# Optimization experiments

Measured on AMD Instinct MI355X. Metric: run time of the kernel, lower is better.

## Reference

```python
import jax, jax.numpy as jnp
import numpy as np

K_DIM = 1024
HEADS = 16


def setup_inputs() -> dict:
    key = jax.random.key(0)
    kx, kw1, kb1, kw2, kb2 = jax.random.split(key, 5)
    b, t, k = 4, 2048, K_DIM
    scale = 1.0 / np.sqrt(k)
    x = jax.random.normal(kx, (b, t, k), dtype=jnp.float32)
    # torch nn.Linear params: weight [out, in], bias [out]
    W_qkv = jax.random.normal(kw1, (3 * k, k), dtype=jnp.float32) * scale
    b_qkv = jax.random.normal(kb1, (3 * k,), dtype=jnp.float32) * scale
    W_out = jax.random.normal(kw2, (k, k), dtype=jnp.float32) * scale
    b_out = jax.random.normal(kb2, (k,), dtype=jnp.float32) * scale
    return {"x": x, "W_qkv": W_qkv, "b_qkv": b_qkv, "W_out": W_out, "b_out": b_out}


def reference(x, W_qkv, b_qkv, W_out, b_out):
    b, t, k = x.shape
    h = HEADS
    s = k // h
    # tokqv linear: [b,t,3k]
    kqv = jnp.einsum('btk,ok->bto', x, W_qkv) + b_qkv
    # view [b,t,h,3s] -> transpose -> [b,h,t,3s], then split q,k,v along last dim
    kqv = kqv.reshape(b, t, h, 3 * s).transpose(0, 2, 1, 3)
    q, kk, v = kqv[..., :s], kqv[..., s:2 * s], kqv[..., 2 * s:]
    scores = jnp.einsum('bhqd,bhkd->bhqk', q, kk) / jnp.sqrt(jnp.float32(s * h))  # note: scale uses full k per source (queries.size(-1)=s, but here head dim s)
    # Faithful: original attention scales by sqrt(queries.size(-1)) = sqrt(s)
    scores = jnp.einsum('bhqd,bhkd->bhqk', q, kk) / jnp.sqrt(jnp.float32(s))
    weights = jax.nn.softmax(scores, axis=-1)
    res = jnp.einsum('bhqk,bhkd->bhqd', weights, v)  # [b,h,t,s]
    res = res.transpose(0, 2, 1, 3).reshape(b, t, k)
    return jnp.einsum('btk,ok->bto', res, W_out) + b_out
```

## Files before the change

### kernel.cpp

```cpp
#include <hip/hip_runtime.h>
#include <hip/hip_bf16.h>

typedef float  f32x4  __attribute__((ext_vector_type(4)));
typedef float  f32x8  __attribute__((ext_vector_type(8)));
typedef float  f32x16 __attribute__((ext_vector_type(16)));
typedef __bf16 bf16x8 __attribute__((ext_vector_type(8)));
typedef unsigned short u16x4 __attribute__((ext_vector_type(4)));
typedef unsigned short u16x8 __attribute__((ext_vector_type(8)));
typedef unsigned int   u32x4 __attribute__((ext_vector_type(4)));

#define QSCALE 0.18033688011112042f

__device__ __forceinline__ unsigned short f2bf(float f) {
  __bf16 h = (__bf16)f;
  return __builtin_bit_cast(unsigned short, h);
}

__device__ __forceinline__ f32x4 mfma16(bf16x8 a, bf16x8 b, f32x4 c) {
  return __builtin_amdgcn_mfma_f32_16x16x32_bf16(a, b, c, 0, 0, 0);
}
__device__ __forceinline__ f32x16 mfma32(bf16x8 a, bf16x8 b, f32x16 c) {
  return __builtin_amdgcn_mfma_f32_32x32x16_bf16(a, b, c, 0, 0, 0);
}
__device__ __forceinline__ f32x16 zero16() {
  f32x16 v;
#pragma unroll
  for (int i = 0; i < 16; ++i) v[i] = 0.f;
  return v;
}

typedef const __attribute__((address_space(1))) void* gptr_t;
typedef __attribute__((address_space(3))) void* lptr_t;
__device__ __forceinline__ void gld16(const void* g, void* l) {
  __builtin_amdgcn_global_load_lds((gptr_t)g, (lptr_t)l, 16, 0, 0);
}


__global__ __launch_bounds__(256) void prep_x(const float* __restrict__ x,
                                              unsigned short* __restrict__ A1) {
  const int mb = blockIdx.x >> 5;
  const int kB = blockIdx.x & 31;
#pragma unroll
  for (int ph = 0; ph < 2; ++ph) {
    int c = threadIdx.x + ph * 256;
    int lg = c >> 7, r = c & 127;
    f32x8 v = *(const f32x8*)(x + (size_t)(mb * 128 + r) * 1024 + kB * 32 + lg * 8);
    u16x8 h;
#pragma unroll
    for (int j = 0; j < 8; ++j) h[j] = f2bf(v[j]);
    *(u16x8*)(A1 + (size_t)(mb * 32 + kB) * 4096 + (size_t)c * 8) = h;
  }
}

__global__ __launch_bounds__(256) void prep_w(const float* __restrict__ w,
                                              unsigned short* __restrict__ o) {
  const int rb = blockIdx.x >> 5;
  const int kB = blockIdx.x & 31;
#pragma unroll
  for (int ph = 0; ph < 2; ++ph) {
    int c = threadIdx.x + ph * 256;
    int lg = c >> 7, r = c & 127;
    f32x8 v = *(const f32x8*)(w + (size_t)(rb * 128 + r) * 1024 + kB * 32 + lg * 8);
    u16x8 h;
#pragma unroll
    for (int j = 0; j < 8; ++j) h[j] = f2bf(v[j]);
    *(u16x8*)(o + (size_t)(rb * 32 + kB) * 4096 + (size_t)c * 8) = h;
  }
}

template <int EPI>
__global__ __launch_bounds__(256, 2) void gemm_bt(
    const __bf16* __restrict__ A, const __bf16* __restrict__ B,
    const float* __restrict__ bias, int N, int nbx, int NT,
    unsigned short* __restrict__ q_out, unsigned short* __restrict__ k_out,
    unsigned short* __restrict__ v_out, float* __restrict__ f_out) {
  __shared__ __align__(16) char smem[3 * 24576];
  const int tid = threadIdx.x;
  const int lane = tid & 63;
  const int wave = tid >> 6;
  const int ln = lane & 15, lg = lane >> 4;
  const int wm = wave >> 1;
  const int wn = wave & 1;
  const int bm = blockIdx.x / nbx;
  const int bn = blockIdx.x % nbx;

  f32x4 acc[8][4];
#pragma unroll
  for (int i = 0; i < 8; ++i)
#pragma unroll
    for (int j = 0; j < 4; ++j) acc[i][j] = (f32x4){0.f, 0.f, 0.f, 0.f};

  const __bf16* Asrc0 = A + ((size_t)(2 * bm) * NT) * 4096 + tid * 8;
  const __bf16* Asrc1 = Asrc0 + (size_t)NT * 4096;
  const __bf16* Bsrc  = B + ((size_t)bn * 32) * 4096 + tid * 8;
  const int aoff = wm * 8192 + lg * 2048 + ln * 16;
  const int boff = 16384 + lg * 2048 + wn * 1024 + ln * 16;

#define STAGE(slot_, tf_)                                                      \
  do {                                                                         \
    char* d_ = smem + (slot_) * 24576;                                         \
    const __bf16* a0_ = Asrc0 + (size_t)(tf_) * 4096;                          \
    const __bf16* a1_ = Asrc1 + (size_t)(tf_) * 4096;                          \
    const __bf16* b_  = Bsrc + (size_t)((tf_) & 31) * 4096;                    \
    gld16(a0_, d_ + tid * 16);                                                 \
    gld16(a0_ + 2048, d_ + 4096 + tid * 16);                                   \
    gld16(a1_, d_ + 8192 + tid * 16);                                          \
    gld16(a1_ + 2048, d_ + 12288 + tid * 16);                                  \
    gld16(b_, d_ + 16384 + tid * 16);                                          \
    gld16(b_ + 2048, d_ + 20480 + tid * 16);                                   \
  } while (0)

#define KBODY(t_, scur_, snxt_)                                                \
  do {                                                                         \
    int tf_ = ((t_) + 2 < NT) ? (t_) + 2 : NT - 1;                             \
    STAGE(snxt_, tf_);                                                         \
    const char* ab_ = smem + (scur_) * 24576;                                  \
    bf16x8 af_[8], bq_[4];                                                     \
    _Pragma("unroll") for (int mi = 0; mi < 8; ++mi)                           \
        af_[mi] = *(const bf16x8*)(ab_ + aoff + mi * 256);                     \
    _Pragma("unroll") for (int ni = 0; ni < 4; ++ni)                           \
        bq_[ni] = *(const bf16x8*)(ab_ + boff + ni * 256);                     \
    __builtin_amdgcn_s_setprio(1);                                             \
    _Pragma("unroll") for (int mi = 0; mi < 8; ++mi)                           \
        _Pragma("unroll") for (int ni = 0; ni < 4; ++ni)                       \
            acc[mi][ni] = mfma16(af_[mi], bq_[ni], acc[mi][ni]);               \
    __builtin_amdgcn_s_setprio(0);                                             \
    asm volatile("s_waitcnt vmcnt(6)\n\ts_barrier" ::: "memory");              \
  } while (0)

  STAGE(0, 0);
  STAGE(1, 1);
  asm volatile("s_waitcnt vmcnt(6)\n\ts_barrier" ::: "memory");

  for (int t = 0; t < NT; t += 3) {
    KBODY(t, 0, 2);
    if (t + 1 < NT) KBODY(t + 1, 1, 0);
    if (t + 2 < NT) KBODY(t + 2, 2, 1);
  }
  asm volatile("s_waitcnt vmcnt(0)" ::: "memory");
#undef KBODY
#undef STAGE

#pragma unroll
  for (int mi = 0; mi < 8; ++mi) {
#pragma unroll
    for (int ni = 0; ni < 4; ++ni) {
      int n = bn * 128 + wn * 64 + ni * 16 + ln;
      float bv = bias[n];
#pragma unroll
      for (int j = 0; j < 4; ++j) {
        int m = bm * 256 + wm * 128 + mi * 16 + lg * 4 + j;
        float val = acc[mi][ni][j] + bv;
        if constexpr (EPI == 0) {
          int h = n / 192;
          int r3 = n - h * 192;
          int b = m >> 11;
          int t = m & 2047;
          size_t base = (size_t)(b * 16 + h) << 17;
          if (r3 < 64) {
            q_out[base + ((size_t)t << 6) + r3] = f2bf(val * QSCALE);
          } else if (r3 < 128) {
            int d = r3 - 64;
            size_t off = base + (size_t)(t >> 6) * 4096 +
                         (size_t)((((t >> 5) & 1) << 2) + (d >> 4)) * 512 +
                         ((d >> 3) & 1) * 256 + (t & 31) * 8 + (d & 7);
            k_out[off] = f2bf(val);
          } else {
            int c = r3 - 128;
            size_t off = base + (size_t)(t >> 6) * 4096 +
                         (size_t)(((c >> 5) << 2) + ((t >> 4) & 3)) * 512 +
                         ((t >> 3) & 1) * 256 + (c & 31) * 8 + (t & 7);
            v_out[off] = f2bf(val);
          }
        } else {
          f_out[(size_t)m * N + n] = val;
        }
      }
    }
  }
}

__global__ __launch_bounds__(256, 3) void attn2(
    const __bf16* __restrict__ Q, const __bf16* __restrict__ Kg,
    const __bf16* __restrict__ Vg, unsigned short* __restrict__ res) {
  __shared__ __align__(16) __bf16 smem[2][8192];
  const int tid = threadIdx.x;
  const int lane = tid & 63;
  const int wq = tid >> 6;
  const int l31 = lane & 31;
  const int hi = lane >> 5;
  const int bh = blockIdx.x & 63;
  const int q0 = (blockIdx.x >> 6) << 7;
  const size_t bh_elem = (size_t)bh << 17;

  const __bf16* Kbh = Kg + bh_elem;
  const __bf16* Vbh = Vg + bh_elem;

  bf16x8 qf[4];
  {
    const __bf16* qrow = Q + bh_elem + ((size_t)(q0 + wq * 32 + l31) << 6) + hi * 8;
#pragma unroll
    for (int ks = 0; ks < 4; ++ks) qf[ks] = *(const bf16x8*)(qrow + ks * 16);
  }
  const u16x8 one8 = {0x3F80, 0x3F80, 0x3F80, 0x3F80,
                      0x3F80, 0x3F80, 0x3F80, 0x3F80};
  const bf16x8 ones = __builtin_bit_cast(bf16x8, one8);

  f32x16 oacc0 = zero16(), oacc1 = zero16(), lacc = zero16();

  {
    char* sb = (char*)smem[0];
#pragma unroll
    for (int it = 0; it < 2; ++it) {
      int idx = tid + it * 256;
      gld16(Kbh + idx * 8, sb + idx * 16);
      gld16(Vbh + idx * 8, sb + 8192 + idx * 16);
    }
  }
  __syncthreads();

  int cur = 0;
  for (int tile = 0; tile < 32; ++tile) {
    if (tile < 31) {
      char* sb = (char*)smem[cur ^ 1];
      const __bf16* kb = Kbh + (size_t)(tile + 1) * 4096;
      const __bf16* vb = Vbh + (size_t)(tile + 1) * 4096;
#pragma unroll
      for (int it = 0; it < 2; ++it) {
        int idx = tid + it * 256;
        gld16(kb + idx * 8, sb + idx * 16);
        gld16(vb + idx * 8, sb + 8192 + idx * 16);
      }
    }
    const char* kbase = (const char*)smem[cur];
    const char* vbase = kbase + 8192;
    const int loff = hi * 512 + l31 * 16;

#pragma unroll
    for (int t2 = 0; t2 < 2; ++t2) {
      f32x16 s = zero16();
#pragma unroll
      for (int ks = 0; ks < 4; ++ks) {
        bf16x8 kf = *(const bf16x8*)(kbase + (t2 * 4 + ks) * 1024 + loff);
        s = mfma32(kf, qf[ks], s);
      }
      float p[16];
#pragma unroll
      for (int r = 0; r < 16; ++r) p[r] = __builtin_amdgcn_exp2f(s[r]);
      unsigned int pk[8], sw[8];
#pragma unroll
      for (int i = 0; i < 8; ++i) {
        pk[i] = ((unsigned int)f2bf(p[2 * i + 1]) << 16) | f2bf(p[2 * i]);
        sw[i] = __shfl_xor(pk[i], 32);
      }
#pragma unroll
      for (int ks2 = 0; ks2 < 2; ++ks2) {
        unsigned int b0 = hi ? sw[ks2 * 4 + 2] : pk[ks2 * 4 + 0];
        unsigned int b1 = hi ? sw[ks2 * 4 + 3] : pk[ks2 * 4 + 1];
        unsigned int b2 = hi ? pk[ks2 * 4 + 2] : sw[ks2 * 4 + 0];
        unsigned int b3 = hi ? pk[ks2 * 4 + 3] : sw[ks2 * 4 + 1];
        u32x4 bw = {b0, b1, b2, b3};
        bf16x8 pb = __builtin_bit_cast(bf16x8, bw);
        int kb2 = t2 * 2 + ks2;
        bf16x8 v0 = *(const bf16x8*)(vbase + (kb2) * 1024 + loff);
        bf16x8 v1 = *(const bf16x8*)(vbase + (4 + kb2) * 1024 + loff);
        lacc  = mfma32(ones, pb, lacc);
        oacc0 = mfma32(v0, pb, oacc0);
        oacc1 = mfma32(v1, pb, oacc1);
      }
    }
    __syncthreads();
    cur ^= 1;
  }

  float rl = __builtin_amdgcn_rcpf(lacc[0]);
  const int b = bh >> 4, h = bh & 15;
  const int r = wq * 32 + l31;
  const int mb = b * 16 + (blockIdx.x >> 6);
  unsigned short* c0 = res + (size_t)(mb * 32 + 2 * h) * 4096 + r * 8 + hi * 4;
#pragma unroll
  for (int g = 0; g < 4; ++g) {
    u16x4 st0, st1;
#pragma unroll
    for (int rr = 0; rr < 4; ++rr) {
      st0[rr] = f2bf(oacc0[g * 4 + rr] * rl);
      st1[rr] = f2bf(oacc1[g * 4 + rr] * rl);
    }
    *(u16x4*)(c0 + g * 1024) = st0;
    *(u16x4*)(c0 + 4096 + g * 1024) = st1;
  }
}

extern "C" void kernel_launch(void* const* d_in, const int* in_sizes, int n_in,
                              void* d_out, int out_size, void* d_ws, size_t ws_size,
                              hipStream_t stream) {
  const float* x    = (const float*)d_in[0];
  const float* Wqkv = (const float*)d_in[1];
  const float* bqkv = (const float*)d_in[2];
  const float* Wout = (const float*)d_in[3];
  const float* bout = (const float*)d_in[4];
  float* out = (float*)d_out;
  char* ws = (char*)d_ws;

  unsigned short* A1 = (unsigned short*)(ws);
  unsigned short* B1 = (unsigned short*)(ws + 50331648);
  unsigned short* Qb = (unsigned short*)(ws + 69206016);
  unsigned short* Kb = (unsigned short*)(ws + 85983232);
  unsigned short* Vb = (unsigned short*)(ws + 102760448);
  unsigned short* Rb = (unsigned short*)(ws + 119537664);
  unsigned short* Wo = (unsigned short*)(ws + 136314880);

  prep_x<<<64 * 32, 256, 0, stream>>>(x, A1);
  prep_w<<<24 * 32, 256, 0, stream>>>(Wqkv, B1);
  prep_w<<<8 * 32, 256, 0, stream>>>(Wout, Wo);

  gemm_bt<0><<<32 * 24, 256, 0, stream>>>((const __bf16*)A1, (const __bf16*)B1,
                                          bqkv, 3072, 24, 32,
                                          Qb, Kb, Vb, nullptr);

  attn2<<<1024, 256, 0, stream>>>((const __bf16*)Qb, (const __bf16*)Kb,
                                  (const __bf16*)Vb, Rb);

  gemm_bt<1><<<32 * 8, 256, 0, stream>>>((const __bf16*)Rb, (const __bf16*)Wo,
                                         bout, 1024, 8, 32,
                                         nullptr, nullptr, nullptr, out);
}
```

Measured before the change: 204.6 us.

## Use 512-thread attention blocks with triple-buffered K/V prefetch

```diff
diff --git a/kernel.cpp b/kernel.cpp
--- a/kernel.cpp
+++ b/kernel.cpp
@@ -180,17 +180,17 @@
   }
 }
 
-__global__ __launch_bounds__(256, 3) void attn2(
+__global__ __launch_bounds__(512, 4) void attn2(
     const __bf16* __restrict__ Q, const __bf16* __restrict__ Kg,
     const __bf16* __restrict__ Vg, unsigned short* __restrict__ res) {
-  __shared__ __align__(16) __bf16 smem[2][8192];
+  __shared__ __align__(16) char smem[3 * 16384];
   const int tid = threadIdx.x;
   const int lane = tid & 63;
   const int wq = tid >> 6;
   const int l31 = lane & 31;
   const int hi = lane >> 5;
   const int bh = blockIdx.x & 63;
-  const int q0 = (blockIdx.x >> 6) << 7;
+  const int q0 = (blockIdx.x >> 6) << 8;
   const size_t bh_elem = (size_t)bh << 17;
 
   const __bf16* Kbh = Kg + bh_elem;
@@ -208,31 +208,24 @@
 
   f32x16 oacc0 = zero16(), oacc1 = zero16(), lacc = zero16();
 
-  {
-    char* sb = (char*)smem[0];
-#pragma unroll
-    for (int it = 0; it < 2; ++it) {
-      int idx = tid + it * 256;
-      gld16(Kbh + idx * 8, sb + idx * 16);
-      gld16(Vbh + idx * 8, sb + 8192 + idx * 16);
-    }
-  }
-  __syncthreads();
-
-  int cur = 0;
+#define AST(slot_, t_)                                                         \
+  do {                                                                         \
+    char* sb_ = smem + (slot_) * 16384;                                        \
+    gld16(Kbh + (size_t)(t_) * 4096 + tid * 8, sb_ + tid * 16);                \
+    gld16(Vbh + (size_t)(t_) * 4096 + tid * 8, sb_ + 8192 + tid * 16);         \
+  } while (0)
+
+  AST(0, 0);
+  AST(1, 1);
+  asm volatile("s_waitcnt vmcnt(2)\n\ts_barrier" ::: "memory");
+
+  int sc = 0;
   for (int tile = 0; tile < 32; ++tile) {
-    if (tile < 31) {
-      char* sb = (char*)smem[cur ^ 1];
-      const __bf16* kb = Kbh + (size_t)(tile + 1) * 4096;
-      const __bf16* vb = Vbh + (size_t)(tile + 1) * 4096;
-#pragma unroll
-      for (int it = 0; it < 2; ++it) {
-        int idx = tid + it * 256;
-        gld16(kb + idx * 8, sb + idx * 16);
-        gld16(vb + idx * 8, sb + 8192 + idx * 16);
-      }
-    }
-    const char* kbase = (const char*)smem[cur];
+    int tf = (tile + 2 < 32) ? tile + 2 : 31;
+    int sn = sc + 2; if (sn >= 3) sn -= 3;
+    AST(sn, tf);
+
+    const char* kbase = smem + sc * 16384;
     const char* vbase = kbase + 8192;
     const int loff = hi * 512 + l31 * 16;
 
@@ -269,14 +262,17 @@
         oacc1 = mfma32(v1, pb, oacc1);
       }
     }
-    __syncthreads();
-    cur ^= 1;
-  }
+    asm volatile("s_waitcnt vmcnt(2)\n\ts_barrier" ::: "memory");
+    sc = (sc + 1 == 3) ? 0 : sc + 1;
+  }
+  asm volatile("s_waitcnt vmcnt(0)" ::: "memory");
+#undef AST
 
   float rl = __builtin_amdgcn_rcpf(lacc[0]);
   const int b = bh >> 4, h = bh & 15;
-  const int r = wq * 32 + l31;
-  const int mb = b * 16 + (blockIdx.x >> 6);
+  const int rloc = wq * 32 + l31;
+  const int mb = b * 16 + (blockIdx.x >> 6) * 2 + (rloc >> 7);
+  const int r = rloc & 127;
   unsigned short* c0 = res + (size_t)(mb * 32 + 2 * h) * 4096 + r * 8 + hi * 4;
 #pragma unroll
   for (int g = 0; g < 4; ++g) {
@@ -318,8 +314,8 @@
                                           bqkv, 3072, 24, 32,
                                           Qb, Kb, Vb, nullptr);
 
-  attn2<<<1024, 256, 0, stream>>>((const __bf16*)Qb, (const __bf16*)Kb,
-                                  (const __bf16*)Vb, Rb);
+  attn2<<<512, 512, 0, stream>>>((const __bf16*)Qb, (const __bf16*)Kb,
+                                 (const __bf16*)Vb, Rb);
 
   gemm_bt<1><<<32 * 8, 256, 0, stream>>>((const __bf16*)Rb, (const __bf16*)Wo,
                                          bout, 1024, 8, 32,
```

New measurement: 195.7 us. 4.3% less time.
